# Performance work log

Measured on AMD Instinct MI355X. Metric: run time of the kernel, lower is better.

The kernel has to match this reference:

```python
import jax, jax.numpy as jnp
import numpy as np

B, D, H = 262144, 32, 64  # batch, q-dim, hidden width (hidden fixed by source)


def _mlp(x, W1, b1, W2, b2, W3, b3):
    h = jax.nn.relu(x @ W1 + b1)
    h = jax.nn.relu(h @ W2 + b2)
    return h @ W3 + b3  # [B, 1] scalar Lagrangian per sample


def setup_inputs() -> dict:
    key = jax.random.key(0)
    ks = jax.random.split(key, 7)
    inputs = jax.random.normal(ks[0], (B, 2 * D), jnp.float32)
    # Glorot-ish init for the 3 Dense layers of the Lagrangian MLP
    W1 = jax.random.normal(ks[1], (2 * D, H), jnp.float32) * (1.0 / np.sqrt(2 * D))
    b1 = jnp.zeros((H,), jnp.float32)
    W2 = jax.random.normal(ks[2], (H, H), jnp.float32) * (1.0 / np.sqrt(H))
    b2 = jnp.zeros((H,), jnp.float32)
    W3 = jax.random.normal(ks[3], (H, 1), jnp.float32) * (1.0 / np.sqrt(H))
    b3 = jnp.zeros((1,), jnp.float32)
    return {"inputs": inputs, "W1": W1, "b1": b1, "W2": W2, "b2": b2, "W3": W3, "b3": b3}


def reference(inputs, W1, b1, W2, b2, W3, b3):
    q, q_dot = jnp.split(inputs, 2, axis=-1)  # each [B, D]

    # TF tape.gradient sums over output elements -> grad of sum(L)
    def L_sum(q_, qd_):
        return jnp.sum(_mlp(jnp.concatenate([q_, qd_], axis=-1), W1, b1, W2, b2, W3, b3))

    dL_dq = jax.grad(L_sum, argnums=0)(q, q_dot)          # [B, D]
    dL_dq_dot = jax.grad(L_sum, argnums=1)                 # fn
    # tape2.gradient(dL_dq_dot, q) == grad_q of sum(dL/dq_dot)
    d_dt_dL_dq_dot = jax.grad(lambda q_: jnp.sum(dL_dq_dot(q_, q_dot)))(q)  # [B, D]
    return d_dt_dL_dq_dot - dL_dq
```

## Files before the change

kernel.cpp:

```cpp
#include <hip/hip_runtime.h>
#include <hip/hip_bf16.h>

#define BATCH     262144
#define TPB       256
#define GRID_MAIN 2048
#define FLAG_CAP  24576
#define EPS1      2.0e-4f
#define EPS2      4.0e-4f

typedef __attribute__((ext_vector_type(8))) short bf16x8;
typedef __attribute__((ext_vector_type(4))) float f32x4;

union FragU { unsigned int u[4]; bf16x8 v; int4 i4; };

__device__ __forceinline__ unsigned short f2bf(float x) {
    __hip_bfloat16 h = __float2bfloat16(x);
    unsigned short u; __builtin_memcpy(&u, &h, 2); return u;
}
__device__ __forceinline__ float bf2f(unsigned short u) {
    unsigned int w = ((unsigned int)u) << 16;
    float f; __builtin_memcpy(&f, &w, 4); return f;
}

__global__ void lnn_prep(const float* __restrict__ W1, const float* __restrict__ b1,
                         const float* __restrict__ W2, const float* __restrict__ b2,
                         const float* __restrict__ W3,
                         unsigned int* __restrict__ W1AH, unsigned int* __restrict__ W1AL,
                         unsigned int* __restrict__ W2AH, unsigned int* __restrict__ W2AL,
                         unsigned int* __restrict__ VA,   unsigned int* __restrict__ W4A,
                         float* __restrict__ B1A, float* __restrict__ B2A,
                         float* __restrict__ W2T, float* __restrict__ W1T32,
                         unsigned int* __restrict__ cnt) {
    const int g = blockIdx.x * blockDim.x + threadIdx.x;
    if (g == 0) *cnt = 0u;

    for (int t = g; t < 8 * 64 * 4; t += 16384) {
        const int idx = t >> 8, lane = (t >> 2) & 63, r = t & 3;
        const int jt = idx >> 1, kc = idx & 1;
        const int row = lane & 15;
        const int k0 = kc * 32 + (lane >> 4) * 8 + 2 * r;
        {
            const int j = jt * 16 + row;
            const float v0 = W1[(k0 + 0) * 64 + j], v1 = W1[(k0 + 1) * 64 + j];
            const unsigned short h0 = f2bf(v0), h1 = f2bf(v1);
            const unsigned short l0 = f2bf(v0 - bf2f(h0)), l1 = f2bf(v1 - bf2f(h1));
            W1AH[t] = (unsigned)h0 | ((unsigned)h1 << 16);
            W1AL[t] = (unsigned)l0 | ((unsigned)l1 << 16);
        }
        {
            const int j2 = jt * 16 + row;
            const float v0 = W2[(k0 + 0) * 64 + j2], v1 = W2[(k0 + 1) * 64 + j2];
            const unsigned short h0 = f2bf(v0), h1 = f2bf(v1);
            const unsigned short l0 = f2bf(v0 - bf2f(h0)), l1 = f2bf(v1 - bf2f(h1));
            W2AH[t] = (unsigned)h0 | ((unsigned)h1 << 16);
            W2AL[t] = (unsigned)l0 | ((unsigned)l1 << 16);
        }
        {
            const int j = jt * 16 + row;
            const float v0 = W3[k0 + 0] * W2[j * 64 + (k0 + 0)];
            const float v1 = W3[k0 + 1] * W2[j * 64 + (k0 + 1)];
            VA[t] = (unsigned)f2bf(v0) | ((unsigned)f2bf(v1) << 16);
        }
        if (idx < 4) {
            const int mt = idx >> 1;
            const int k = mt * 16 + row;
            const float v0 = -W1[k * 64 + (k0 + 0)], v1 = -W1[k * 64 + (k0 + 1)];
            W4A[t] = (unsigned)f2bf(v0) | ((unsigned)f2bf(v1) << 16);
        }
    }
    for (int t = g; t < 4 * 64 * 4; t += 16384) {
        const int jt = t >> 8, lane = (t >> 2) & 63, r = t & 3;
        const int j = jt * 16 + (lane >> 4) * 4 + r;
        B1A[t] = b1[j];
        B2A[t] = b2[j];
    }
    for (int t = g; t < 64 * 64; t += 16384) {
        const int i = t >> 6, j = t & 63;
        W2T[j * 64 + i] = W2[i * 64 + j];
    }
    for (int t = g; t < 64 * 32; t += 16384) {
        const int i = t >> 5, k = t & 31;
        W1T32[i * 32 + k] = W1[k * 64 + i];
    }
}

__global__ __launch_bounds__(TPB) void lnn_mfma(
        const float* __restrict__ X,
        const unsigned int* __restrict__ W1AH, const unsigned int* __restrict__ W1AL,
        const unsigned int* __restrict__ W2AH, const unsigned int* __restrict__ W2AL,
        const unsigned int* __restrict__ VA,   const unsigned int* __restrict__ W4A,
        const float* __restrict__ B1A, const float* __restrict__ B2A,
        unsigned int* __restrict__ cnt, unsigned int* __restrict__ flagIdx,
        float* __restrict__ out) {
    __shared__ unsigned int  HB[4][64][33];
    __shared__ unsigned short MU[4][64][33];

    const int tid = threadIdx.x;
    const int w  = tid >> 6;
    const int l  = tid & 63;
    const int lr = l & 15;
    const int lg = l >> 4;
    const int s0 = blockIdx.x * 128 + w * 32;

    const f32x4 zz = {0.f, 0.f, 0.f, 0.f};
    f32x4 acc[4][2];

#pragma unroll
    for (int jt = 0; jt < 4; ++jt)
#pragma unroll
        for (int nt = 0; nt < 2; ++nt) acc[jt][nt] = zz;

#pragma unroll
    for (int kc = 0; kc < 2; ++kc) {
        FragU bh[2], bl[2];
#pragma unroll
        for (int nt = 0; nt < 2; ++nt) {
            const float* xp = X + (size_t)(s0 + nt * 16 + lr) * 64 + kc * 32 + lg * 8;
            const float4 x0 = reinterpret_cast<const float4*>(xp)[0];
            const float4 x1 = reinterpret_cast<const float4*>(xp)[1];
            const float xs[8] = {x0.x, x0.y, x0.z, x0.w, x1.x, x1.y, x1.z, x1.w};
#pragma unroll
            for (int r = 0; r < 4; ++r) {
                const unsigned short h0 = f2bf(xs[2 * r]),     h1 = f2bf(xs[2 * r + 1]);
                const unsigned short q0 = f2bf(xs[2 * r] - bf2f(h0));
                const unsigned short q1 = f2bf(xs[2 * r + 1] - bf2f(h1));
                bh[nt].u[r] = (unsigned)h0 | ((unsigned)h1 << 16);
                bl[nt].u[r] = (unsigned)q0 | ((unsigned)q1 << 16);
            }
        }
#pragma unroll
        for (int jt = 0; jt < 4; ++jt) {
            FragU ah, al;
            ah.i4 = reinterpret_cast<const int4*>(W1AH)[(jt * 2 + kc) * 64 + l];
            al.i4 = reinterpret_cast<const int4*>(W1AL)[(jt * 2 + kc) * 64 + l];
#pragma unroll
            for (int nt = 0; nt < 2; ++nt) {
                acc[jt][nt] = __builtin_amdgcn_mfma_f32_16x16x32_bf16(al.v, bh[nt].v, acc[jt][nt], 0, 0, 0);
                acc[jt][nt] = __builtin_amdgcn_mfma_f32_16x16x32_bf16(ah.v, bl[nt].v, acc[jt][nt], 0, 0, 0);
                acc[jt][nt] = __builtin_amdgcn_mfma_f32_16x16x32_bf16(ah.v, bh[nt].v, acc[jt][nt], 0, 0, 0);
            }
        }
    }

    unsigned int m1 = 0u;
#pragma unroll
    for (int jt = 0; jt < 4; ++jt) {
        const float4 bv = reinterpret_cast<const float4*>(B1A)[jt * 64 + l];
        const float bb[4] = {bv.x, bv.y, bv.z, bv.w};
#pragma unroll
        for (int nt = 0; nt < 2; ++nt) {
            const int sc = nt * 16 + lr;
#pragma unroll
            for (int r = 0; r < 4; ++r) {
                const float z = acc[jt][nt][r] + bb[r];
                if (z > 0.f) m1 |= 1u << (jt * 8 + nt * 4 + r);
                if (__builtin_fabsf(z) < EPS1) {
                    const unsigned int pos = atomicAdd(cnt, 1u);
                    if (pos < FLAG_CAP) flagIdx[pos] = (unsigned int)(s0 + sc);
                }
                const float h = fmaxf(z, 0.f);
                const unsigned short hh = f2bf(h);
                const unsigned short hl = f2bf(h - bf2f(hh));
                HB[w][jt * 16 + lg * 4 + r][sc] = (unsigned)hh | ((unsigned)hl << 16);
            }
        }
    }

#pragma unroll
    for (int jt = 0; jt < 4; ++jt)
#pragma unroll
        for (int nt = 0; nt < 2; ++nt) acc[jt][nt] = zz;

#pragma unroll
    for (int kc = 0; kc < 2; ++kc) {
        FragU bh[2], bl[2];
#pragma unroll
        for (int nt = 0; nt < 2; ++nt) {
            const int sc = nt * 16 + lr;
#pragma unroll
            for (int r = 0; r < 4; ++r) {
                const int i0 = kc * 32 + lg * 8 + 2 * r;
                const unsigned int ue = HB[w][i0][sc];
                const unsigned int uo = HB[w][i0 + 1][sc];
                bh[nt].u[r] = (ue & 0xFFFFu) | (uo << 16);
                bl[nt].u[r] = (ue >> 16) | (uo & 0xFFFF0000u);
            }
        }
#pragma unroll
        for (int jt = 0; jt < 4; ++jt) {
            FragU ah, al;
            ah.i4 = reinterpret_cast<const int4*>(W2AH)[(jt * 2 + kc) * 64 + l];
            al.i4 = reinterpret_cast<const int4*>(W2AL)[(jt * 2 + kc) * 64 + l];
#pragma unroll
            for (int nt = 0; nt < 2; ++nt) {
                acc[jt][nt] = __builtin_amdgcn_mfma_f32_16x16x32_bf16(al.v, bh[nt].v, acc[jt][nt], 0, 0, 0);
                acc[jt][nt] = __builtin_amdgcn_mfma_f32_16x16x32_bf16(ah.v, bl[nt].v, acc[jt][nt], 0, 0, 0);
                acc[jt][nt] = __builtin_amdgcn_mfma_f32_16x16x32_bf16(ah.v, bh[nt].v, acc[jt][nt], 0, 0, 0);
            }
        }
    }

#pragma unroll
    for (int jt = 0; jt < 4; ++jt) {
        const float4 bv = reinterpret_cast<const float4*>(B2A)[jt * 64 + l];
        const float bb[4] = {bv.x, bv.y, bv.z, bv.w};
#pragma unroll
        for (int nt = 0; nt < 2; ++nt) {
            const int sc = nt * 16 + lr;
#pragma unroll
            for (int r = 0; r < 4; ++r) {
                const float z = acc[jt][nt][r] + bb[r];
                MU[w][jt * 16 + lg * 4 + r][sc] = (z > 0.f) ? (unsigned short)0x3F80u
                                                            : (unsigned short)0u;
                if (__builtin_fabsf(z) < EPS2) {
                    const unsigned int pos = atomicAdd(cnt, 1u);
                    if (pos < FLAG_CAP) flagIdx[pos] = (unsigned int)(s0 + sc);
                }
            }
        }
    }

#pragma unroll
    for (int jt = 0; jt < 4; ++jt)
#pragma unroll
        for (int nt = 0; nt < 2; ++nt) acc[jt][nt] = zz;

#pragma unroll
    for (int kc = 0; kc < 2; ++kc) {
        FragU bm[2];
#pragma unroll
        for (int nt = 0; nt < 2; ++nt) {
            const int sc = nt * 16 + lr;
#pragma unroll
            for (int r = 0; r < 4; ++r) {
                const int i0 = kc * 32 + lg * 8 + 2 * r;
                const unsigned int ue = MU[w][i0][sc];
                const unsigned int uo = MU[w][i0 + 1][sc];
                bm[nt].u[r] = ue | (uo << 16);
            }
        }
#pragma unroll
        for (int jt = 0; jt < 4; ++jt) {
            FragU av;
            av.i4 = reinterpret_cast<const int4*>(VA)[(jt * 2 + kc) * 64 + l];
#pragma unroll
            for (int nt = 0; nt < 2; ++nt)
                acc[jt][nt] = __builtin_amdgcn_mfma_f32_16x16x32_bf16(av.v, bm[nt].v, acc[jt][nt], 0, 0, 0);
        }
    }
#pragma unroll
    for (int jt = 0; jt < 4; ++jt)
#pragma unroll
        for (int nt = 0; nt < 2; ++nt) {
            const int sc = nt * 16 + lr;
#pragma unroll
            for (int r = 0; r < 4; ++r) {
                const float uv = ((m1 >> (jt * 8 + nt * 4 + r)) & 1u) ? acc[jt][nt][r] : 0.f;
                MU[w][jt * 16 + lg * 4 + r][sc] = f2bf(uv);
            }
        }

    f32x4 acc4[2][2];
#pragma unroll
    for (int mt = 0; mt < 2; ++mt)
#pragma unroll
        for (int nt = 0; nt < 2; ++nt) acc4[mt][nt] = zz;

#pragma unroll
    for (int kc = 0; kc < 2; ++kc) {
        FragU bu[2];
#pragma unroll
        for (int nt = 0; nt < 2; ++nt) {
            const int sc = nt * 16 + lr;
#pragma unroll
            for (int r = 0; r < 4; ++r) {
                const int i0 = kc * 32 + lg * 8 + 2 * r;
                const unsigned int ue = MU[w][i0][sc];
                const unsigned int uo = MU[w][i0 + 1][sc];
                bu[nt].u[r] = ue | (uo << 16);
            }
        }
#pragma unroll
        for (int mt = 0; mt < 2; ++mt) {
            FragU a4;
            a4.i4 = reinterpret_cast<const int4*>(W4A)[(mt * 2 + kc) * 64 + l];
#pragma unroll
            for (int nt = 0; nt < 2; ++nt)
                acc4[mt][nt] = __builtin_amdgcn_mfma_f32_16x16x32_bf16(a4.v, bu[nt].v, acc4[mt][nt], 0, 0, 0);
        }
    }
#pragma unroll
    for (int mt = 0; mt < 2; ++mt)
#pragma unroll
        for (int nt = 0; nt < 2; ++nt)
#pragma unroll
            for (int r = 0; r < 4; ++r)
                out[(size_t)(s0 + nt * 16 + lr) * 32 + mt * 16 + lg * 4 + r] = acc4[mt][nt][r];
}

__global__ __launch_bounds__(64) void lnn_repair(
        const float* __restrict__ X,
        const float* __restrict__ W1, const float* __restrict__ b1,
        const float* __restrict__ W2, const float* __restrict__ b2,
        const float* __restrict__ W3, const float* __restrict__ W2T,
        const float* __restrict__ W1T32,
        const unsigned int* __restrict__ cnt, const unsigned int* __restrict__ flagIdx,
        float* __restrict__ out) {
    const int l = threadIdx.x;
    int n = (int)*cnt;
    if (n > FLAG_CAP) n = FLAG_CAP;

    for (int idx = blockIdx.x; idx < n; idx += gridDim.x) {
        const int s = (int)flagIdx[idx];
        const float xv = X[(size_t)s * 64 + l];

        float z1 = 0.f;
        for (int i = 0; i < 64; ++i)
            z1 = fmaf(__shfl(xv, i), W1[i * 64 + l], z1);
        z1 += b1[l];
        const unsigned long long m1 = __ballot(z1 > 0.f);
        const float h = fmaxf(z1, 0.f);

        float z2 = 0.f;
        for (int i = 0; i < 64; ++i)
            z2 = fmaf(__shfl(h, i), W2[i * 64 + l], z2);
        z2 += b2[l];
        const unsigned long long m2 = __ballot(z2 > 0.f);

        float t = 0.f;
        for (int j2 = 0; j2 < 64; ++j2)
            if ((m2 >> j2) & 1ull) t = fmaf(W3[j2], W2T[j2 * 64 + l], t);
        const float u = ((m1 >> l) & 1ull) ? t : 0.f;

        float o = 0.f;
        for (int i = 0; i < 64; ++i)
            o = fmaf(__shfl(u, i), (l < 32) ? W1T32[i * 32 + l] : 0.f, o);
        if (l < 32) out[(size_t)s * 32 + l] = -o;
    }
}

extern "C" void kernel_launch(void* const* d_in, const int* in_sizes, int n_in,
                              void* d_out, int out_size, void* d_ws, size_t ws_size,
                              hipStream_t stream) {
    const float* X  = (const float*)d_in[0];
    const float* W1 = (const float*)d_in[1];
    const float* b1 = (const float*)d_in[2];
    const float* W2 = (const float*)d_in[3];
    const float* b2 = (const float*)d_in[4];
    const float* W3 = (const float*)d_in[5];
    float* out = (float*)d_out;

    char* ws = (char*)d_ws;
    unsigned int* W1AH = (unsigned int*)(ws + 0);
    unsigned int* W1AL = (unsigned int*)(ws + 8192);
    unsigned int* W2AH = (unsigned int*)(ws + 16384);
    unsigned int* W2AL = (unsigned int*)(ws + 24576);
    unsigned int* VAp  = (unsigned int*)(ws + 32768);
    unsigned int* W4Ap = (unsigned int*)(ws + 40960);
    float*        B1A  = (float*)(ws + 45056);
    float*        B2A  = (float*)(ws + 49152);
    float*        W2T  = (float*)(ws + 53248);
    float*        W1T32= (float*)(ws + 69632);
    unsigned int* CNT  = (unsigned int*)(ws + 77824);
    unsigned int* FIDX = (unsigned int*)(ws + 77840);

    lnn_prep<<<64, 256, 0, stream>>>(W1, b1, W2, b2, W3,
                                     W1AH, W1AL, W2AH, W2AL, VAp, W4Ap,
                                     B1A, B2A, W2T, W1T32, CNT);
    lnn_mfma<<<GRID_MAIN, TPB, 0, stream>>>(X, W1AH, W1AL, W2AH, W2AL, VAp, W4Ap,
                                            B1A, B2A, CNT, FIDX, out);
    lnn_repair<<<2048, 64, 0, stream>>>(X, W1, b1, W2, b2, W3, W2T, W1T32,
                                        CNT, FIDX, out);
}
```

Measured before the change: 284.7 us.

## Fuse fp32 repair pass into MFMA kernel using per-wave ballot flag masks

Removes the separate repair kernel and global atomic flag list. Near-threshold samples are now marked with a wave-ballot bitmask, and the same wave recomputes them in fp32 right after its MFMA output, skipping stores for flagged rows. The HB and MU shared buffers are merged into one aliased allocation, which cuts LDS use and may raise occupancy. In exchange, the per-sample repair loop now runs inside the main kernel and can cause wave divergence or tail imbalance, and it adds code size and register pressure.

```diff
diff --git a/kernel.cpp b/kernel.cpp
--- a/kernel.cpp
+++ b/kernel.cpp
@@ -4,7 +4,6 @@
 #define BATCH     262144
 #define TPB       256
 #define GRID_MAIN 2048
-#define FLAG_CAP  24576
 #define EPS1      2.0e-4f
 #define EPS2      4.0e-4f
 
@@ -20,6 +19,10 @@
 __device__ __forceinline__ float bf2f(unsigned short u) {
     unsigned int w = ((unsigned int)u) << 16;
     float f; __builtin_memcpy(&f, &w, 4); return f;
+}
+__device__ __forceinline__ unsigned int fold16(unsigned long long b) {
+    b |= b >> 32; b |= b >> 16;
+    return (unsigned int)(b & 0xFFFFull);
 }
 
 __global__ void lnn_prep(const float* __restrict__ W1, const float* __restrict__ b1,
@@ -29,10 +32,8 @@
                          unsigned int* __restrict__ W2AH, unsigned int* __restrict__ W2AL,
                          unsigned int* __restrict__ VA,   unsigned int* __restrict__ W4A,
                          float* __restrict__ B1A, float* __restrict__ B2A,
-                         float* __restrict__ W2T, float* __restrict__ W1T32,
-                         unsigned int* __restrict__ cnt) {
+                         float* __restrict__ W2T, float* __restrict__ W1T32) {
     const int g = blockIdx.x * blockDim.x + threadIdx.x;
-    if (g == 0) *cnt = 0u;
 
     for (int t = g; t < 8 * 64 * 4; t += 16384) {
         const int idx = t >> 8, lane = (t >> 2) & 63, r = t & 3;
@@ -90,10 +91,12 @@
         const unsigned int* __restrict__ W2AH, const unsigned int* __restrict__ W2AL,
         const unsigned int* __restrict__ VA,   const unsigned int* __restrict__ W4A,
         const float* __restrict__ B1A, const float* __restrict__ B2A,
-        unsigned int* __restrict__ cnt, unsigned int* __restrict__ flagIdx,
+        const float* __restrict__ W1, const float* __restrict__ b1,
+        const float* __restrict__ W2, const float* __restrict__ b2,
+        const float* __restrict__ W3, const float* __restrict__ W2T,
+        const float* __restrict__ W1T32,
         float* __restrict__ out) {
-    __shared__ unsigned int  HB[4][64][33];
-    __shared__ unsigned short MU[4][64][33];
+    __shared__ unsigned int SMEM[4][64 * 33];
 
     const int tid = threadIdx.x;
     const int w  = tid >> 6;
@@ -102,8 +105,12 @@
     const int lg = l >> 4;
     const int s0 = blockIdx.x * 128 + w * 32;
 
+    unsigned int* __restrict__ HBw = SMEM[w];
+    unsigned short* __restrict__ MUw = (unsigned short*)SMEM[w];
+
     const f32x4 zz = {0.f, 0.f, 0.f, 0.f};
     f32x4 acc[4][2];
+    unsigned int flagmask = 0u;
 
 #pragma unroll
     for (int jt = 0; jt < 4; ++jt)
@@ -143,27 +150,30 @@
     }
 
     unsigned int m1 = 0u;
-#pragma unroll
-    for (int jt = 0; jt < 4; ++jt) {
-        const float4 bv = reinterpret_cast<const float4*>(B1A)[jt * 64 + l];
-        const float bb[4] = {bv.x, bv.y, bv.z, bv.w};
-#pragma unroll
-        for (int nt = 0; nt < 2; ++nt) {
-            const int sc = nt * 16 + lr;
-#pragma unroll
-            for (int r = 0; r < 4; ++r) {
-                const float z = acc[jt][nt][r] + bb[r];
-                if (z > 0.f) m1 |= 1u << (jt * 8 + nt * 4 + r);
-                if (__builtin_fabsf(z) < EPS1) {
-                    const unsigned int pos = atomicAdd(cnt, 1u);
-                    if (pos < FLAG_CAP) flagIdx[pos] = (unsigned int)(s0 + sc);
+    {
+        bool f0 = false, f1 = false;
+#pragma unroll
+        for (int jt = 0; jt < 4; ++jt) {
+            const float4 bv = reinterpret_cast<const float4*>(B1A)[jt * 64 + l];
+            const float bb[4] = {bv.x, bv.y, bv.z, bv.w};
+#pragma unroll
+            for (int nt = 0; nt < 2; ++nt) {
+                const int sc = nt * 16 + lr;
+#pragma unroll
+                for (int r = 0; r < 4; ++r) {
+                    const float z = acc[jt][nt][r] + bb[r];
+                    if (z > 0.f) m1 |= 1u << (jt * 8 + nt * 4 + r);
+                    const bool c = __builtin_fabsf(z) < EPS1;
+                    if (nt == 0) f0 |= c; else f1 |= c;
+                    const float h = fmaxf(z, 0.f);
+                    const unsigned short hh = f2bf(h);
+                    const unsigned short hl = f2bf(h - bf2f(hh));
+                    HBw[(jt * 16 + lg * 4 + r) * 33 + sc] = (unsigned)hh | ((unsigned)hl << 16);
                 }
-                const float h = fmaxf(z, 0.f);
-                const unsigned short hh = f2bf(h);
-                const unsigned short hl = f2bf(h - bf2f(hh));
-                HB[w][jt * 16 + lg * 4 + r][sc] = (unsigned)hh | ((unsigned)hl << 16);
-            }
-        }
+            }
+        }
+        flagmask |= fold16(__ballot(f0));
+        flagmask |= fold16(__ballot(f1)) << 16;
     }
 
 #pragma unroll
@@ -180,8 +190,8 @@
 #pragma unroll
             for (int r = 0; r < 4; ++r) {
                 const int i0 = kc * 32 + lg * 8 + 2 * r;
-                const unsigned int ue = HB[w][i0][sc];
-                const unsigned int uo = HB[w][i0 + 1][sc];
+                const unsigned int ue = HBw[i0 * 33 + sc];
+                const unsigned int uo = HBw[(i0 + 1) * 33 + sc];
                 bh[nt].u[r] = (ue & 0xFFFFu) | (uo << 16);
                 bl[nt].u[r] = (ue >> 16) | (uo & 0xFFFF0000u);
             }
@@ -200,24 +210,27 @@
         }
     }
 
-#pragma unroll
-    for (int jt = 0; jt < 4; ++jt) {
-        const float4 bv = reinterpret_cast<const float4*>(B2A)[jt * 64 + l];
-        const float bb[4] = {bv.x, bv.y, bv.z, bv.w};
-#pragma unroll
-        for (int nt = 0; nt < 2; ++nt) {
-            const int sc = nt * 16 + lr;
-#pragma unroll
-            for (int r = 0; r < 4; ++r) {
-                const float z = acc[jt][nt][r] + bb[r];
-                MU[w][jt * 16 + lg * 4 + r][sc] = (z > 0.f) ? (unsigned short)0x3F80u
-                                                            : (unsigned short)0u;
-                if (__builtin_fabsf(z) < EPS2) {
-                    const unsigned int pos = atomicAdd(cnt, 1u);
-                    if (pos < FLAG_CAP) flagIdx[pos] = (unsigned int)(s0 + sc);
+    {
+        bool f0 = false, f1 = false;
+#pragma unroll
+        for (int jt = 0; jt < 4; ++jt) {
+            const float4 bv = reinterpret_cast<const float4*>(B2A)[jt * 64 + l];
+            const float bb[4] = {bv.x, bv.y, bv.z, bv.w};
+#pragma unroll
+            for (int nt = 0; nt < 2; ++nt) {
+                const int sc = nt * 16 + lr;
+#pragma unroll
+                for (int r = 0; r < 4; ++r) {
+                    const float z = acc[jt][nt][r] + bb[r];
+                    MUw[(jt * 16 + lg * 4 + r) * 33 + sc] =
+                        (z > 0.f) ? (unsigned short)0x3F80u : (unsigned short)0u;
+                    const bool c = __builtin_fabsf(z) < EPS2;
+                    if (nt == 0) f0 |= c; else f1 |= c;
                 }
             }
         }
+        flagmask |= fold16(__ballot(f0));
+        flagmask |= fold16(__ballot(f1)) << 16;
     }
 
 #pragma unroll
@@ -234,8 +247,8 @@
 #pragma unroll
             for (int r = 0; r < 4; ++r) {
                 const int i0 = kc * 32 + lg * 8 + 2 * r;
-                const unsigned int ue = MU[w][i0][sc];
-                const unsigned int uo = MU[w][i0 + 1][sc];
+                const unsigned int ue = MUw[i0 * 33 + sc];
+                const unsigned int uo = MUw[(i0 + 1) * 33 + sc];
                 bm[nt].u[r] = ue | (uo << 16);
             }
         }
@@ -256,7 +269,7 @@
 #pragma unroll
             for (int r = 0; r < 4; ++r) {
                 const float uv = ((m1 >> (jt * 8 + nt * 4 + r)) & 1u) ? acc[jt][nt][r] : 0.f;
-                MU[w][jt * 16 + lg * 4 + r][sc] = f2bf(uv);
+                MUw[(jt * 16 + lg * 4 + r) * 33 + sc] = f2bf(uv);
             }
         }
 
@@ -275,8 +288,8 @@
 #pragma unroll
             for (int r = 0; r < 4; ++r) {
                 const int i0 = kc * 32 + lg * 8 + 2 * r;
-                const unsigned int ue = MU[w][i0][sc];
-                const unsigned int uo = MU[w][i0 + 1][sc];
+                const unsigned int ue = MUw[i0 * 33 + sc];
+                const unsigned int uo = MUw[(i0 + 1) * 33 + sc];
                 bu[nt].u[r] = ue | (uo << 16);
             }
         }
@@ -292,49 +305,47 @@
 #pragma unroll
     for (int mt = 0; mt < 2; ++mt)
 #pragma unroll
-        for (int nt = 0; nt < 2; ++nt)
+        for (int nt = 0; nt < 2; ++nt) {
+            const bool keep = !((flagmask >> (nt * 16 + lr)) & 1u);
 #pragma unroll
             for (int r = 0; r < 4; ++r)
-                out[(size_t)(s0 + nt * 16 + lr) * 32 + mt * 16 + lg * 4 + r] = acc4[mt][nt][r];
-}
-
-__global__ __launch_bounds__(64) void lnn_repair(
-        const float* __restrict__ X,
-        const float* __restrict__ W1, const float* __restrict__ b1,
-        const float* __restrict__ W2, const float* __restrict__ b2,
-        const float* __restrict__ W3, const float* __restrict__ W2T,
-        const float* __restrict__ W1T32,
-        const unsigned int* __restrict__ cnt, const unsigned int* __restrict__ flagIdx,
-        float* __restrict__ out) {
-    const int l = threadIdx.x;
-    int n = (int)*cnt;
-    if (n > FLAG_CAP) n = FLAG_CAP;
-
-    for (int idx = blockIdx.x; idx < n; idx += gridDim.x) {
-        const int s = (int)flagIdx[idx];
+                if (keep)
+                    out[(size_t)(s0 + nt * 16 + lr) * 32 + mt * 16 + lg * 4 + r] = acc4[mt][nt][r];
+        }
+
+    unsigned int fm = flagmask;
+    while (fm) {
+        const int sc = __ffs(fm) - 1; fm &= fm - 1;
+        const int s = s0 + sc;
         const float xv = X[(size_t)s * 64 + l];
 
         float z1 = 0.f;
+#pragma unroll 1
         for (int i = 0; i < 64; ++i)
             z1 = fmaf(__shfl(xv, i), W1[i * 64 + l], z1);
         z1 += b1[l];
-        const unsigned long long m1 = __ballot(z1 > 0.f);
+        const unsigned long long m1r = __ballot(z1 > 0.f);
         const float h = fmaxf(z1, 0.f);
 
         float z2 = 0.f;
+#pragma unroll 1
         for (int i = 0; i < 64; ++i)
             z2 = fmaf(__shfl(h, i), W2[i * 64 + l], z2);
         z2 += b2[l];
-        const unsigned long long m2 = __ballot(z2 > 0.f);
-
-        float t = 0.f;
+        const unsigned long long m2r = __ballot(z2 > 0.f);
+
+        float tv = 0.f;
+#pragma unroll 1
         for (int j2 = 0; j2 < 64; ++j2)
-            if ((m2 >> j2) & 1ull) t = fmaf(W3[j2], W2T[j2 * 64 + l], t);
-        const float u = ((m1 >> l) & 1ull) ? t : 0.f;
+            if ((m2r >> j2) & 1ull) tv = fmaf(W3[j2], W2T[j2 * 64 + l], tv);
+        const float uv = ((m1r >> l) & 1ull) ? tv : 0.f;
 
         float o = 0.f;
-        for (int i = 0; i < 64; ++i)
-            o = fmaf(__shfl(u, i), (l < 32) ? W1T32[i * 32 + l] : 0.f, o);
+#pragma unroll 1
+        for (int i = 0; i < 64; ++i) {
+            const float wv = (l < 32) ? W1T32[i * 32 + l] : 0.f;
+            o = fmaf(__shfl(uv, i), wv, o);
+        }
         if (l < 32) out[(size_t)s * 32 + l] = -o;
     }
 }
@@ -361,14 +372,11 @@
     float*        B2A  = (float*)(ws + 49152);
     float*        W2T  = (float*)(ws + 53248);
     float*        W1T32= (float*)(ws + 69632);
-    unsigned int* CNT  = (unsigned int*)(ws + 77824);
-    unsigned int* FIDX = (unsigned int*)(ws + 77840);
 
     lnn_prep<<<64, 256, 0, stream>>>(W1, b1, W2, b2, W3,
                                      W1AH, W1AL, W2AH, W2AL, VAp, W4Ap,
-                                     B1A, B2A, W2T, W1T32, CNT);
+                                     B1A, B2A, W2T, W1T32);
     lnn_mfma<<<GRID_MAIN, TPB, 0, stream>>>(X, W1AH, W1AL, W2AH, W2AL, VAp, W4Ap,
-                                            B1A, B2A, CNT, FIDX, out);
-    lnn_repair<<<2048, 64, 0, stream>>>(X, W1, b1, W2, b2, W3, W2T, W1T32,
-                                        CNT, FIDX, out);
-}
+                                            B1A, B2A, W1, b1, W2, b2, W3, W2T, W1T32,
+                                            out);
+}
```

Result: slower. 361.4 us (+26.9%).
